# Optimization experiments

Hardware: AMD Instinct MI355X
Metric: run time of the kernel (lower is better)

The kernel has to match this reference:

```python
import jax, jax.numpy as jnp
import numpy as np

D_MODEL, D_INNER, D_STATE, D_CONV, NHEADS, HEADDIM, CHUNK = 2048, 4096, 128, 4, 64, 64, 64
CONV_DIM = D_INNER + 2 * D_STATE  # 4352
D_IN_PROJ = 2 * D_INNER + 2 * D_STATE + NHEADS  # 8512
EPS = 1e-5

def setup_inputs() -> dict:
    key = jax.random.key(0)
    ks = jax.random.split(key, 8)
    B, L = 2, 4096
    return {
        'u': jax.random.normal(ks[0], (B, L, D_MODEL), jnp.float32),
        'W_in': jax.random.normal(ks[1], (D_IN_PROJ, D_MODEL), jnp.float32) * 0.02,
        'conv_w': jax.random.normal(ks[2], (CONV_DIM, D_CONV), jnp.float32) * 0.2,
        'conv_b': jax.random.normal(ks[3], (CONV_DIM,), jnp.float32) * 0.02,
        'dt_bias': jax.random.normal(ks[4], (NHEADS,), jnp.float32) * 0.5,
        'A_log': jax.random.normal(ks[5], (NHEADS,), jnp.float32) * 0.5,
        'D': jax.random.normal(ks[6], (NHEADS,), jnp.float32),
        'norm_w': jnp.ones((D_INNER,), jnp.float32),
        'W_out': jax.random.normal(ks[7], (D_MODEL, D_INNER), jnp.float32) * 0.02,
    }

def silu(x):
    return x * jax.nn.sigmoid(x)

def segsum(x):
    # x: (..., T) -> (..., T, T); out[..., i, j] = sum_{j < k <= i} x[..., k], -inf above diag
    T = x.shape[-1]
    xr = jnp.broadcast_to(x[..., None], x.shape + (T,))
    m1 = jnp.tril(jnp.ones((T, T), bool), -1)
    s = jnp.cumsum(jnp.where(m1, xr, 0.0), axis=-2)
    m0 = jnp.tril(jnp.ones((T, T), bool), 0)
    return jnp.where(m0, s, -jnp.inf)

def ssd(x, A, B, C, chunk):
    # x: (b,L,h,p)  A: (b,L,h)  B,C: (b,L,n) shared across heads
    b, L, h, p = x.shape
    c = L // chunk
    x = x.reshape(b, c, chunk, h, p)
    A = A.reshape(b, c, chunk, h).transpose(0, 3, 1, 2)  # b h c l
    B = B.reshape(b, c, chunk, -1)
    C = C.reshape(b, c, chunk, -1)
    A_cs = jnp.cumsum(A, axis=-1)
    Lmat = jnp.exp(segsum(A))  # (b,h,c,l,s)
    Y_diag = jnp.einsum('bcln,bcsn,bhcls,bcshp->bclhp', C, B, Lmat, x)
    decay_states = jnp.exp(A_cs[..., -1:] - A_cs)  # (b,h,c,l)
    states = jnp.einsum('bcln,bhcl,bclhp->bchpn', B, decay_states, x)
    states = jnp.concatenate([jnp.zeros_like(states[:, :1]), states], axis=1)
    A_last = jnp.pad(A_cs[..., -1], ((0, 0), (0, 0), (1, 0)))  # (b,h,c+1)
    decay_chunk = jnp.exp(segsum(A_last))  # (b,h,c+1,c+1)
    new_states = jnp.einsum('bhzc,bchpn->bzhpn', decay_chunk, states)
    states, final = new_states[:, :-1], new_states[:, -1]
    sdo = jnp.exp(A_cs)  # (b,h,c,l)
    Y_off = jnp.einsum('bcln,bchpn,bhcl->bclhp', C, states, sdo)
    return (Y_diag + Y_off).reshape(b, L, h, p), final

def reference(u, W_in, conv_w, conv_b, dt_bias, A_log, D, norm_w, W_out):
    b, L, _ = u.shape
    zxbcdt = jnp.einsum('bld,ed->ble', u, W_in)
    z = zxbcdt[..., :D_INNER]
    xBC = zxbcdt[..., D_INNER:D_INNER + CONV_DIM]
    dt = jax.nn.softplus(zxbcdt[..., -NHEADS:] + dt_bias)  # (b,L,h)
    A = -jnp.exp(A_log)
    da_log = dt * A  # (b,L,h)
    # causal depthwise conv1d (kernel D_CONV, left pad D_CONV-1)
    xp = jnp.pad(xBC, ((0, 0), (D_CONV - 1, 0), (0, 0)))
    xBC = sum(xp[:, k:k + L, :] * conv_w[:, k] for k in range(D_CONV)) + conv_b
    xBC = silu(xBC)
    x = xBC[..., :D_INNER].reshape(b, L, NHEADS, HEADDIM)
    Bm = xBC[..., D_INNER:D_INNER + D_STATE]
    Cm = xBC[..., D_INNER + D_STATE:]
    y, final_state = ssd(x * dt[..., None], da_log, Bm, Cm, CHUNK)
    y = y + x * D[None, None, :, None]
    y = y.reshape(b, L, D_INNER)
    y = y * silu(z)
    y = y * jax.lax.rsqrt(jnp.mean(y * y, axis=-1, keepdims=True) + EPS) * norm_w
    return jnp.einsum('bld,ed->ble', y, W_out)
```

## Files before the change

### kernel.cpp

```cpp
#include <hip/hip_runtime.h>
#include <stdint.h>
#include <stddef.h>

#define SEQ     4096
#define DMODEL  2048
#define DINNER  4096
#define DSTATE  128
#define NH      64
#define HD      64
#define NCHUNK  64
#define CONVDIM 4352
#define DPROJ   8512

typedef __bf16 bf16_t;
typedef __bf16 bf16x8 __attribute__((ext_vector_type(8)));
typedef float  f32x4  __attribute__((ext_vector_type(4)));

__device__ __forceinline__ void async_cp16(const bf16_t* g, bf16_t* l) {
    __builtin_amdgcn_global_load_lds(
        (const __attribute__((address_space(1))) void*)g,
        (__attribute__((address_space(3))) void*)l,
        16, 0, 0);
}

__global__ __launch_bounds__(256) void zero_out_kernel(float* out, int n) {
    int i = blockIdx.x*256 + threadIdx.x;
    if (i < n) out[i] = 0.f;
}

__global__ void detect_kernel(const unsigned short* norm_w_raw, int* flag) {
    if (threadIdx.x == 0 && blockIdx.x == 0)
        *flag = (norm_w_raw[0] == 0x3F80) ? 1 : 0;
}

__global__ __launch_bounds__(256) void cast_kernel(
    const void* __restrict__ src, size_t elem_off, bf16_t* __restrict__ dst,
    int n, const int* __restrict__ flag)
{
    int i = blockIdx.x*256 + threadIdx.x;
    if (i >= n) return;
    if (*flag) dst[i] = ((const bf16_t*)src)[elem_off + i];
    else       dst[i] = (bf16_t)(((const float*)src)[elem_off + i]);
}

__device__ __forceinline__ void stage_half(
    const bf16_t* __restrict__ G, int grow0, int gmaxrow, int gld,
    int kt, bf16_t* lplane, int half, int tid)
{
    #pragma unroll
    for (int q = 0; q < 2; q++) {
        int rloc = half*128 + q*64 + (tid >> 3);
        int grow = grow0 + rloc; if (grow > gmaxrow) grow = gmaxrow;
        int gcol = kt + ((((tid & 7) ^ (rloc & 7))) << 3);
        async_cp16(G + (size_t)grow*gld + gcol, lplane + rloc*64 + ((tid & 7) << 3));
    }
}

#define GMM_READ_A(PLANE, KS)                                                  \
    _Pragma("unroll")                                                          \
    for (int m_ = 0; m_ < 8; m_++) {                                           \
        const int rl_ = wmBase + m_*16 + lrow;                                 \
        afr[m_] = *(const bf16x8*)((PLANE) + rl_*64 + ((((KS)*4+quad) ^ (rl_&7))<<3)); \
    }

#define GMM_READ_B(PLANE, KS, DST)                                             \
    _Pragma("unroll")                                                          \
    for (int n_ = 0; n_ < 4; n_++) {                                           \
        const int rl_ = wnBase + n_*16 + lrow;                                 \
        DST[n_] = *(const bf16x8*)((PLANE) + rl_*64 + ((((KS)*4+quad) ^ (rl_&7))<<3)); \
    }

#define GMM_TAIL(BKARR, NA, NB)                                                \
    __builtin_amdgcn_s_barrier();                                              \
    asm volatile("s_waitcnt lgkmcnt(0)" ::: "memory");                         \
    __builtin_amdgcn_sched_barrier(0);                                         \
    __builtin_amdgcn_s_setprio(1);                                             \
    _Pragma("unroll")                                                          \
    for (int m_ = 0; m_ < 8; m_++) {                                           \
        acc[m_][NA] = __builtin_amdgcn_mfma_f32_16x16x32_bf16(afr[m_], BKARR[NA], acc[m_][NA], 0,0,0); \
        acc[m_][NB] = __builtin_amdgcn_mfma_f32_16x16x32_bf16(afr[m_], BKARR[NB], acc[m_][NB], 0,0,0); \
    }                                                                          \
    __builtin_amdgcn_s_setprio(0);

template <typename OT>
__global__ __launch_bounds__(512, 2) void gemm256_kernel(
    const bf16_t* __restrict__ A, const bf16_t* __restrict__ W,
    OT* __restrict__ C, int M, int N, int K, int lda)
{
    extern __shared__ __align__(16) bf16_t lds[];
    bf16_t* lAa = lds;
    bf16_t* lAb = lds + 16384;
    bf16_t* lBa = lds + 32768;
    bf16_t* lBb = lds + 49152;

    const int tid  = threadIdx.x;
    const int lane = tid & 63;
    const int wid  = tid >> 6;
    const int lrow = lane & 15;
    const int quad = lane >> 4;
    const int wmBase = (wid >> 2) * 128;
    const int wnBase = (wid & 3) * 64;

    int wg = blockIdx.x;
    const int nwg = gridDim.x;
    if ((nwg & 7) == 0) { int cpx = nwg >> 3; wg = (wg & 7)*cpx + (wg >> 3); }
    const int ntx = (N + 255) >> 8;
    const int n0 = (wg % ntx) * 256;
    const int m0 = (wg / ntx) * 256;

    const int NT   = K >> 6;
    const int NTm1 = NT - 1;
    const int NT2  = NT >> 1;

    f32x4 acc[8][4] = {};
    bf16x8 afr[8], bk0[4], bk1[4];

    stage_half(A, m0, M-1, lda, 0,  lAa, 0, tid);
    stage_half(A, m0, M-1, lda, 0,  lAa, 1, tid);
    stage_half(W, n0, N-1, K,   0,  lBa, 0, tid);
    stage_half(W, n0, N-1, K,   0,  lBa, 1, tid);
    stage_half(A, m0, M-1, lda, 64, lAb, 0, tid);
    asm volatile("s_waitcnt vmcnt(2)" ::: "memory");
    __builtin_amdgcn_s_barrier();

    for (int i = 0; i < NT2; i++) {
        const int ktb = (2*i + 1) * 64;
        const int ktc = ((2*i + 2) & NTm1) * 64;
        const int ktd = ((2*i + 3) & NTm1) * 64;

        GMM_READ_A(lAa, 0)
        GMM_READ_B(lBa, 0, bk0)
        stage_half(A, m0, M-1, lda, ktb, lAb, 1, tid);
        GMM_TAIL(bk0, 0, 1)
        __builtin_amdgcn_s_barrier();
        GMM_READ_B(lBa, 1, bk1)
        stage_half(W, n0, N-1, K, ktb, lBb, 0, tid);
        GMM_TAIL(bk0, 2, 3)
        __builtin_amdgcn_s_barrier();
        GMM_READ_A(lAa, 1)
        stage_half(W, n0, N-1, K, ktb, lBb, 1, tid);
        GMM_TAIL(bk1, 0, 1)
        __builtin_amdgcn_s_barrier();
        stage_half(A, m0, M-1, lda, ktc, lAa, 0, tid);
        GMM_TAIL(bk1, 2, 3)
        asm volatile("s_waitcnt vmcnt(2)" ::: "memory");
        __builtin_amdgcn_s_barrier();

        GMM_READ_A(lAb, 0)
        GMM_READ_B(lBb, 0, bk0)
        stage_half(A, m0, M-1, lda, ktc, lAa, 1, tid);
        GMM_TAIL(bk0, 0, 1)
        __builtin_amdgcn_s_barrier();
        GMM_READ_B(lBb, 1, bk1)
        stage_half(W, n0, N-1, K, ktc, lBa, 0, tid);
        GMM_TAIL(bk0, 2, 3)
        __builtin_amdgcn_s_barrier();
        GMM_READ_A(lAb, 1)
        stage_half(W, n0, N-1, K, ktc, lBa, 1, tid);
        GMM_TAIL(bk1, 0, 1)
        __builtin_amdgcn_s_barrier();
        stage_half(A, m0, M-1, lda, ktd, lAb, 0, tid);
        GMM_TAIL(bk1, 2, 3)
        asm volatile("s_waitcnt vmcnt(2)" ::: "memory");
        __builtin_amdgcn_s_barrier();
    }

    asm volatile("s_waitcnt vmcnt(0)" ::: "memory");

    #pragma unroll
    for (int m = 0; m < 8; m++) {
        const int row = m0 + wmBase + m*16 + quad*4;
        #pragma unroll
        for (int n = 0; n < 4; n++) {
            const int col = n0 + wnBase + n*16 + lrow;
            if (col < N) {
                #pragma unroll
                for (int rr = 0; rr < 4; rr++)
                    C[(size_t)(row + rr)*N + col] = (OT)acc[m][n][rr];
            }
        }
    }
}

__global__ __launch_bounds__(256) void dt_kernel(
    const bf16_t* __restrict__ zx, const bf16_t* __restrict__ dt_bias,
    float* __restrict__ dtb)
{
    int i = blockIdx.x*256 + threadIdx.x;
    int h = i & 63, row = i >> 6;
    float raw = (float)zx[(size_t)row*DPROJ + (DINNER + CONVDIM) + h] + (float)dt_bias[h];
    dtb[i] = (raw > 20.f) ? raw : log1pf(expf(raw));
}

__global__ void cumsum_kernel(
    const float* __restrict__ dtb, const bf16_t* __restrict__ A_log,
    float* __restrict__ Acs)
{
    int blk = blockIdx.x;
    int h = blk & 63, c = blk >> 6;
    int lane = threadIdx.x;
    float Ah = -expf((float)A_log[h]);
    size_t row = (size_t)c*64 + lane;
    float v = dtb[row*64 + h] * Ah;
    #pragma unroll
    for (int off = 1; off < 64; off <<= 1) {
        float t = __shfl_up(v, off, 64);
        if (lane >= off) v += t;
    }
    Acs[(size_t)blk*64 + lane] = v;
}

__global__ __launch_bounds__(256) void conv_kernel(
    const bf16_t* __restrict__ zx, const bf16_t* __restrict__ conv_w,
    const bf16_t* __restrict__ conv_b, bf16_t* __restrict__ xbc)
{
    int i = blockIdx.x*256 + threadIdx.x;
    int cb = i % (CONVDIM/8);
    int l  = i / (CONVDIM/8);
    int ch0 = cb*8;
    const bf16_t* src = zx + (size_t)l*DPROJ + DINNER + ch0;
    float acc[8];
    {
        bf16x8 bv = *(const bf16x8*)(conv_b + ch0);
        #pragma unroll
        for (int j = 0; j < 8; j++) acc[j] = (float)bv[j];
    }
    bf16x8 w4[4];
    #pragma unroll
    for (int t = 0; t < 4; t++) w4[t] = *(const bf16x8*)(conv_w + ch0*4 + t*8);
    #pragma unroll
    for (int k = 0; k < 4; k++) {
        int ll = l - 3 + k;
        if (ll >= 0) {
            bf16x8 v = *(const bf16x8*)(src + (ptrdiff_t)(k-3)*DPROJ);
            #pragma unroll
            for (int j = 0; j < 8; j++)
                acc[j] += (float)v[j] * (float)w4[(j*4+k)>>3][(j*4+k)&7];
        }
    }
    bf16x8 o;
    #pragma unroll
    for (int j = 0; j < 8; j++)
        o[j] = (bf16_t)(acc[j] / (1.f + expf(-acc[j])));
    *(bf16x8*)(xbc + (size_t)i*8) = o;
}

__global__ __launch_bounds__(256) void states_kernel(
    const bf16_t* __restrict__ xbc, const float* __restrict__ dtb,
    const float* __restrict__ Acs, bf16_t* __restrict__ states)
{
    __shared__ __align__(16) bf16_t XsT[64*64];
    __shared__ __align__(16) bf16_t BT[128*64];
    __shared__ float AcsS[64];
    __shared__ float scaleS[64];
    const int blk = blockIdx.x;
    const int h = blk & 63, c = blk >> 6;
    const int tid = threadIdx.x, lane = tid & 63, wid = tid >> 6;
    const size_t rowbase = (size_t)c*64;

    if (tid < 64) AcsS[tid] = Acs[(size_t)blk*64 + tid];
    __syncthreads();
    if (tid < 64) scaleS[tid] = dtb[(rowbase + tid)*64 + h] * expf(AcsS[63] - AcsS[tid]);
    __syncthreads();

    {
        bf16x8 xa[2], b0[2], b1[2];
        #pragma unroll
        for (int half = 0; half < 2; half++) {
            #pragma unroll
            for (int j = 0; j < 8; j++) {
                int l = wid*16 + half*8 + j;
                const bf16_t* rp = xbc + (rowbase + l)*CONVDIM;
                xa[half][j] = (bf16_t)((float)rp[h*64 + lane] * scaleS[l]);
                b0[half][j] = rp[DINNER + lane];
                b1[half][j] = rp[DINNER + 64 + lane];
            }
        }
        #pragma unroll
        for (int half = 0; half < 2; half++) {
            int cch = wid*2 + half;
            *(bf16x8*)(XsT + lane*64       + ((cch ^ (lane & 7))*8)) = xa[half];
            *(bf16x8*)(BT  + lane*64       + ((cch ^ (lane & 7))*8)) = b0[half];
            *(bf16x8*)(BT  + (lane+64)*64  + ((cch ^ (lane & 7))*8)) = b1[half];
        }
    }
    __syncthreads();

    const int lrow = lane & 15, quad = lane >> 4;
    const int waveM = (wid & 1) * 32;
    const int waveN = (wid >> 1) * 64;
    f32x4 acc[2][4] = {};
    #pragma unroll
    for (int ks = 0; ks < 2; ks++) {
        bf16x8 af[2], bfr[4];
        #pragma unroll
        for (int i = 0; i < 2; i++) {
            int p = waveM + i*16 + lrow;
            af[i] = *(const bf16x8*)(XsT + p*64 + (((ks*4 + quad) ^ (p & 7))*8));
        }
        #pragma unroll
        for (int j = 0; j < 4; j++) {
            int n = waveN + j*16 + lrow;
            bfr[j] = *(const bf16x8*)(BT + n*64 + (((ks*4 + quad) ^ (n & 7))*8));
        }
        #pragma unroll
        for (int i = 0; i < 2; i++)
            #pragma unroll
            for (int j = 0; j < 4; j++)
                acc[i][j] = __builtin_amdgcn_mfma_f32_16x16x32_bf16(af[i], bfr[j], acc[i][j], 0, 0, 0);
    }

    const size_t sbase = (size_t)blk*8192;
    #pragma unroll
    for (int i = 0; i < 2; i++)
        #pragma unroll
        for (int j = 0; j < 4; j++) {
            int n = waveN + j*16 + lrow;
            #pragma unroll
            for (int r = 0; r < 4; r++) {
                int p = waveM + i*16 + quad*4 + r;
                states[sbase + (size_t)p*128 + n] = (bf16_t)acc[i][j][r];
            }
        }
}

__global__ __launch_bounds__(256) void gmat_kernel(
    const bf16_t* __restrict__ xbc, float* __restrict__ Gt)
{
    __shared__ __align__(16) float Ct[128*64];
    __shared__ __align__(16) float Bs2[64*128];
    int c = blockIdx.x;
    int tid = threadIdx.x;
    size_t rowbase = (size_t)c*64;
    for (int e = tid; e < 8192; e += 256) {
        int l = e >> 7, n = e & 127;
        const bf16_t* rp = xbc + (rowbase + l)*CONVDIM + DINNER;
        Bs2[e] = (float)rp[n];
        Ct[n*64 + (l ^ (n & 63))] = (float)rp[128 + n];
    }
    __syncthreads();
    int l = tid & 63, s0 = (tid >> 6) * 16;
    float acc[16] = {};
    for (int n4 = 0; n4 < 128; n4 += 4) {
        float c0 = Ct[(n4+0)*64 + (l ^ ((n4+0) & 63))];
        float c1 = Ct[(n4+1)*64 + (l ^ ((n4+1) & 63))];
        float c2 = Ct[(n4+2)*64 + (l ^ ((n4+2) & 63))];
        float c3 = Ct[(n4+3)*64 + (l ^ ((n4+3) & 63))];
        #pragma unroll
        for (int j = 0; j < 16; j++) {
            f32x4 bv = *(const f32x4*)&Bs2[(s0+j)*128 + n4];
            acc[j] += c0*bv[0] + c1*bv[1] + c2*bv[2] + c3*bv[3];
        }
    }
    float* gp = Gt + (size_t)c*4096;
    #pragma unroll
    for (int j = 0; j < 16; j++) gp[l*64 + (s0+j)] = acc[j];
}

__global__ __launch_bounds__(256) void scan_kernel(
    bf16_t* __restrict__ states, const float* __restrict__ Acs)
{
    int i = blockIdx.x*256 + threadIdx.x;
    int n = i & 127, p = (i >> 7) & 63, h = i >> 13;
    size_t off = (size_t)h*8192 + (size_t)p*128 + n;
    const float* ac = Acs + (size_t)h*64 + 63;
    float S = 0.f;
    for (int c = 0; c < 64; c++) {
        float tmp = (float)states[off];
        states[off] = (bf16_t)S;
        S = expf(ac[(size_t)c*4096]) * S + tmp;
        off += (size_t)64*8192;
    }
}

__global__ __launch_bounds__(256) void y_kernel(
    const bf16_t* __restrict__ xbc, const float* __restrict__ dtb,
    const float* __restrict__ Acs, const float* __restrict__ Gt,
    const bf16_t* __restrict__ states, const bf16_t* __restrict__ Dvec,
    bf16_t* __restrict__ y)
{
    __shared__ __align__(16) bf16_t Cs[64*128];
    __shared__ __align__(16) bf16_t Ss[64*128];
    __shared__ __align__(16) bf16_t Wm[64*64];
    __shared__ __align__(16) bf16_t XdT[64*64];
    __shared__ float acsS[64];
    __shared__ float dtS[64];
    const int blk = blockIdx.x;
    const int h = blk & 63, c = blk >> 6;
    const int tid = threadIdx.x, lane = tid & 63, wid = tid >> 6;
    const size_t rowbase = (size_t)c*64;
    const size_t sbase = (size_t)blk*8192;

    if (tid < 64) {
        acsS[tid] = Acs[(size_t)blk*64 + tid];
        dtS[tid]  = dtb[(rowbase + tid)*64 + h];
    }
    __syncthreads();

    #pragma unroll
    for (int it = 0; it < 4; it++) {
        int q = wid*256 + it*64 + lane;
        int l = q >> 4;
        int cl = (q & 15) ^ (l & 7);
        async_cp16(xbc + (rowbase + l)*CONVDIM + DINNER + 128 + cl*8,
                   Cs + (size_t)(wid*256 + it*64)*8);
        async_cp16(states + sbase + (size_t)l*128 + cl*8,
                   Ss + (size_t)(wid*256 + it*64)*8);
    }

    {
        const float* gp = Gt + (size_t)c*4096;
        #pragma unroll
        for (int k = 0; k < 16; k++) {
            int e = k*256 + tid;
            int l = e >> 6, s = e & 63;
            float w = 0.f;
            if (s <= l) w = gp[e] * expf(acsS[l] - acsS[s]);
            Wm[l*64 + (((s >> 3) ^ (l & 7))*8) + (s & 7)] = (bf16_t)w;
        }
    }

    {
        bf16x8 xd[2];
        #pragma unroll
        for (int half = 0; half < 2; half++)
            #pragma unroll
            for (int j = 0; j < 8; j++) {
                int s = wid*16 + half*8 + j;
                xd[half][j] = (bf16_t)((float)xbc[(rowbase + s)*CONVDIM + h*64 + lane] * dtS[s]);
            }
        #pragma unroll
        for (int half = 0; half < 2; half++) {
            int cch = wid*2 + half;
            *(bf16x8*)(XdT + lane*64 + ((cch ^ (lane & 7))*8)) = xd[half];
        }
    }
    __syncthreads();

    const int lrow = lane & 15, quad = lane >> 4;
    const int waveM = (wid & 1) * 32;
    const int waveN = (wid >> 1) * 32;
    f32x4 acc[2][2] = {};

    #pragma unroll
    for (int ks = 0; ks < 4; ks++) {
        bf16x8 af[2], bfr[2];
        #pragma unroll
        for (int i = 0; i < 2; i++) {
            int l = waveM + i*16 + lrow;
            af[i] = *(const bf16x8*)(Cs + l*128 + (((ks*4 + quad) ^ (l & 7))*8));
        }
        #pragma unroll
        for (int j = 0; j < 2; j++) {
            int p = waveN + j*16 + lrow;
            bfr[j] = *(const bf16x8*)(Ss + p*128 + (((ks*4 + quad) ^ (p & 7))*8));
        }
        #pragma unroll
        for (int i = 0; i < 2; i++)
            #pragma unroll
            for (int j = 0; j < 2; j++)
                acc[i][j] = __builtin_amdgcn_mfma_f32_16x16x32_bf16(af[i], bfr[j], acc[i][j], 0, 0, 0);
    }

    #pragma unroll
    for (int i = 0; i < 2; i++)
        #pragma unroll
        for (int r = 0; r < 4; r++) {
            int l = waveM + i*16 + quad*4 + r;
            float el = expf(acsS[l]);
            #pragma unroll
            for (int j = 0; j < 2; j++)
                acc[i][j][r] *= el;
        }

    #pragma unroll
    for (int ks = 0; ks < 2; ks++) {
        bf16x8 af[2], bfr[2];
        #pragma unroll
        for (int i = 0; i < 2; i++) {
            int l = waveM + i*16 + lrow;
            af[i] = *(const bf16x8*)(Wm + l*64 + (((ks*4 + quad) ^ (l & 7))*8));
        }
        #pragma unroll
        for (int j = 0; j < 2; j++) {
            int p = waveN + j*16 + lrow;
            bfr[j] = *(const bf16x8*)(XdT + p*64 + (((ks*4 + quad) ^ (p & 7))*8));
        }
        #pragma unroll
        for (int i = 0; i < 2; i++)
            #pragma unroll
            for (int j = 0; j < 2; j++)
                acc[i][j] = __builtin_amdgcn_mfma_f32_16x16x32_bf16(af[i], bfr[j], acc[i][j], 0, 0, 0);
    }

    const float Dh = (float)Dvec[h];
    #pragma unroll
    for (int i = 0; i < 2; i++)
        #pragma unroll
        for (int r = 0; r < 4; r++) {
            int l = waveM + i*16 + quad*4 + r;
            const bf16_t* xr = xbc + (rowbase + l)*CONVDIM + h*64;
            bf16_t* yr = y + (rowbase + l)*DPROJ + h*64;
            #pragma unroll
            for (int j = 0; j < 2; j++) {
                int p = waveN + j*16 + lrow;
                yr[p] = (bf16_t)(acc[i][j][r] + Dh * (float)xr[p]);
            }
        }
}

__global__ __launch_bounds__(256) void gatenorm_kernel(
    bf16_t* __restrict__ zx, const bf16_t* __restrict__ norm_w)
{
    __shared__ float red[4];
    int row = blockIdx.x;
    int tid = threadIdx.x;
    const bf16_t* zr = zx + (size_t)row*DPROJ;
    bf16_t* yr = zx + (size_t)row*DPROJ + DINNER;
    float vals[16]; float ss = 0.f;
    #pragma unroll
    for (int i = 0; i < 16; i++) {
        int e = i*256 + tid;
        float zv = (float)zr[e];
        float g = (float)yr[e] * (zv / (1.f + expf(-zv)));
        vals[i] = g; ss += g*g;
    }
    #pragma unroll
    for (int off = 32; off >= 1; off >>= 1) ss += __shfl_down(ss, off, 64);
    if ((tid & 63) == 0) red[tid >> 6] = ss;
    __syncthreads();
    float tot = red[0] + red[1] + red[2] + red[3];
    float scale = rsqrtf(tot * (1.f/4096.f) + 1e-5f);
    #pragma unroll
    for (int i = 0; i < 16; i++) {
        int e = i*256 + tid;
        yr[e] = (bf16_t)(vals[i] * scale * (float)norm_w[e]);
    }
}

extern "C" void kernel_launch(void* const* d_in, const int* in_sizes, int n_in,
                              void* d_out, int out_size, void* d_ws, size_t ws_size,
                              hipStream_t stream)
{
    const void* u_raw      = d_in[0];
    const void* W_in_raw   = d_in[1];
    const void* conv_w_raw = d_in[2];
    const void* conv_b_raw = d_in[3];
    const void* dt_b_raw   = d_in[4];
    const void* A_log_raw  = d_in[5];
    const void* D_raw      = d_in[6];
    const void* norm_w_raw = d_in[7];
    const void* W_out_raw  = d_in[8];
    float* out = (float*)d_out;

    const size_t SZ_HDR = 256 + 65536;
    const size_t SZ_ZX  = (size_t)SEQ*DPROJ*2;
    const size_t SZ_XBC = (size_t)SEQ*CONVDIM*2;
    const size_t SZ_ST  = (size_t)4096*8192*2;
    const size_t SZ_DTB = (size_t)SEQ*64*4;
    const size_t SZ_ACS = (size_t)4096*64*4;
    const size_t SZ_GT  = (size_t)64*4096*4;
    const size_t REQ = SZ_HDR + SZ_ZX + SZ_XBC + SZ_ST + SZ_DTB + SZ_ACS + SZ_GT;

    if (ws_size < REQ) {
        zero_out_kernel<<<(out_size + 255)/256, 256, 0, stream>>>(out, out_size);
        return;
    }

    static int smem_set = 0;
    if (!smem_set) {
        hipFuncSetAttribute(reinterpret_cast<const void*>(gemm256_kernel<bf16_t>),
                            hipFuncAttributeMaxDynamicSharedMemorySize, 131072);
        hipFuncSetAttribute(reinterpret_cast<const void*>(gemm256_kernel<float>),
                            hipFuncAttributeMaxDynamicSharedMemorySize, 131072);
        smem_set = 1;
    }

    char* w = (char*)d_ws;
    int*    flag   = (int*)w;            w += 256;
    bf16_t* smallb = (bf16_t*)w;         w += 65536;
    bf16_t* zx     = (bf16_t*)w;         w += SZ_ZX;
    bf16_t* xbc    = (bf16_t*)w;         w += SZ_XBC;
    bf16_t* states = (bf16_t*)w;         w += SZ_ST;
    float*  dtb    = (float*)w;          w += SZ_DTB;
    float*  Acs    = (float*)w;          w += SZ_ACS;
    float*  Gt     = (float*)w;          w += SZ_GT;
    bf16_t* yb     = zx + DINNER;

    bf16_t* conv_w_b  = smallb;
    bf16_t* conv_b_b  = smallb + 17408;
    bf16_t* dt_bias_b = smallb + 21760;
    bf16_t* A_log_b   = smallb + 21824;
    bf16_t* D_b       = smallb + 21888;
    bf16_t* norm_w_b  = smallb + 21952;
    bf16_t* u_b    = states;
    bf16_t* W_in_b = states + (size_t)SEQ*DMODEL;
    bf16_t* W_out_b = states;

    dim3 blk(256);
    detect_kernel<<<1, 1, 0, stream>>>((const unsigned short*)norm_w_raw, flag);
    cast_kernel<<<(17408+255)/256, blk, 0, stream>>>(conv_w_raw, 0, conv_w_b, 17408, flag);
    cast_kernel<<<(4352+255)/256,  blk, 0, stream>>>(conv_b_raw, 0, conv_b_b, 4352, flag);
    cast_kernel<<<1,               blk, 0, stream>>>(dt_b_raw,   0, dt_bias_b, 64, flag);
    cast_kernel<<<1,               blk, 0, stream>>>(A_log_raw,  0, A_log_b, 64, flag);
    cast_kernel<<<1,               blk, 0, stream>>>(D_raw,      0, D_b, 64, flag);
    cast_kernel<<<16,              blk, 0, stream>>>(norm_w_raw, 0, norm_w_b, 4096, flag);

    for (int b = 0; b < 2; b++) {
        float* outb = out + (size_t)b*SEQ*DMODEL;
        cast_kernel<<<32768, blk, 0, stream>>>(u_raw, (size_t)b*SEQ*DMODEL, u_b, SEQ*DMODEL, flag);
        cast_kernel<<<68096, blk, 0, stream>>>(W_in_raw, 0, W_in_b, DPROJ*DMODEL, flag);
        gemm256_kernel<bf16_t><<<dim3(34*16), dim3(512), 131072, stream>>>(
            u_b, W_in_b, zx, SEQ, DPROJ, DMODEL, DMODEL);
        dt_kernel<<<1024, blk, 0, stream>>>(zx, dt_bias_b, dtb);
        cumsum_kernel<<<4096, 64, 0, stream>>>(dtb, A_log_b, Acs);
        conv_kernel<<<8704, blk, 0, stream>>>(zx, conv_w_b, conv_b_b, xbc);
        states_kernel<<<4096, blk, 0, stream>>>(xbc, dtb, Acs, states);
        gmat_kernel<<<64, blk, 0, stream>>>(xbc, Gt);
        scan_kernel<<<2048, blk, 0, stream>>>(states, Acs);
        y_kernel<<<4096, blk, 0, stream>>>(xbc, dtb, Acs, Gt, states, D_b, yb);
        cast_kernel<<<32768, blk, 0, stream>>>(W_out_raw, 0, W_out_b, DMODEL*DINNER, flag);
        gatenorm_kernel<<<4096, blk, 0, stream>>>(zx, norm_w_b);
        gemm256_kernel<float><<<dim3(8*16), dim3(512), 131072, stream>>>(
            yb, W_out_b, outb, SEQ, DMODEL, DINNER, DPROJ);
    }
}
```

Before: 1.151 ms.

## Vectorize casts, split-K the output GEMM, and add partial LDS wait

The scalar cast kernels are replaced by a 4-wide vectorized cast, so each thread moves 16 bytes. The output projection GEMM, which had only 128 tiles, now splits K in two across 256 workgroups to fill more CUs. The second half goes to a float scratch buffer that reuses the xbc region, and a new add kernel sums it into the output. An early partial lgkmcnt wait is also inserted before the first MFMA tail, which may overlap LDS reads with compute; the split-K path costs extra global traffic for the partial sums.

Result: faster. 1.053 ms (-8.5%).

```diff
diff --git a/kernel.cpp b/kernel.cpp
--- a/kernel.cpp
+++ b/kernel.cpp
@@ -15,6 +15,7 @@
 typedef __bf16 bf16_t;
 typedef __bf16 bf16x8 __attribute__((ext_vector_type(8)));
 typedef float  f32x4  __attribute__((ext_vector_type(4)));
+typedef unsigned short u16x4 __attribute__((ext_vector_type(4)));
 
 __device__ __forceinline__ void async_cp16(const bf16_t* g, bf16_t* l) {
     __builtin_amdgcn_global_load_lds(
@@ -41,6 +42,35 @@
     if (i >= n) return;
     if (*flag) dst[i] = ((const bf16_t*)src)[elem_off + i];
     else       dst[i] = (bf16_t)(((const float*)src)[elem_off + i]);
+}
+
+__global__ __launch_bounds__(256) void cast4_kernel(
+    const void* __restrict__ src, size_t elem_off, bf16_t* __restrict__ dst,
+    int n4, const int* __restrict__ flag)
+{
+    int i = blockIdx.x*256 + threadIdx.x;
+    if (i >= n4) return;
+    if (*flag) {
+        u16x4 v = *(const u16x4*)((const unsigned short*)src + elem_off + (size_t)i*4);
+        *(u16x4*)(dst + (size_t)i*4) = v;
+    } else {
+        f32x4 v = *(const f32x4*)((const float*)src + elem_off + (size_t)i*4);
+        bf16_t o[4];
+        #pragma unroll
+        for (int j = 0; j < 4; j++) o[j] = (bf16_t)v[j];
+        *(u16x4*)(dst + (size_t)i*4) = *(const u16x4*)o;
+    }
+}
+
+__global__ __launch_bounds__(256) void addp_kernel(
+    float* __restrict__ out, const float* __restrict__ part, int n4)
+{
+    int i = blockIdx.x*256 + threadIdx.x;
+    if (i >= n4) return;
+    f32x4 a = *(const f32x4*)(out + (size_t)i*4);
+    f32x4 b = *(const f32x4*)(part + (size_t)i*4);
+    a[0]+=b[0]; a[1]+=b[1]; a[2]+=b[2]; a[3]+=b[3];
+    *(f32x4*)(out + (size_t)i*4) = a;
 }
 
 __device__ __forceinline__ void stage_half(
@@ -85,7 +115,7 @@
 template <typename OT>
 __global__ __launch_bounds__(512, 2) void gemm256_kernel(
     const bf16_t* __restrict__ A, const bf16_t* __restrict__ W,
-    OT* __restrict__ C, int M, int N, int K, int lda)
+    OT* C, OT* C2, int M, int N, int K, int lda, int khalf2)
 {
     extern __shared__ __align__(16) bf16_t lds[];
     bf16_t* lAa = lds;
@@ -104,11 +134,21 @@
     int wg = blockIdx.x;
     const int nwg = gridDim.x;
     if ((nwg & 7) == 0) { int cpx = nwg >> 3; wg = (wg & 7)*cpx + (wg >> 3); }
+
+    const int wld = K;
+    int kloc = K;
+    OT* Cw = C;
+    if (khalf2) {
+        const int htiles = nwg >> 1;
+        kloc = K >> 1;
+        if (wg >= htiles) { Cw = C2; wg -= htiles; A += kloc; W += kloc; }
+    }
+
     const int ntx = (N + 255) >> 8;
     const int n0 = (wg % ntx) * 256;
     const int m0 = (wg / ntx) * 256;
 
-    const int NT   = K >> 6;
+    const int NT   = kloc >> 6;
     const int NTm1 = NT - 1;
     const int NT2  = NT >> 1;
 
@@ -117,8 +157,8 @@
 
     stage_half(A, m0, M-1, lda, 0,  lAa, 0, tid);
     stage_half(A, m0, M-1, lda, 0,  lAa, 1, tid);
-    stage_half(W, n0, N-1, K,   0,  lBa, 0, tid);
-    stage_half(W, n0, N-1, K,   0,  lBa, 1, tid);
+    stage_half(W, n0, N-1, wld, 0,  lBa, 0, tid);
+    stage_half(W, n0, N-1, wld, 0,  lBa, 1, tid);
     stage_half(A, m0, M-1, lda, 64, lAb, 0, tid);
     asm volatile("s_waitcnt vmcnt(2)" ::: "memory");
     __builtin_amdgcn_s_barrier();
@@ -131,14 +171,15 @@
         GMM_READ_A(lAa, 0)
         GMM_READ_B(lBa, 0, bk0)
         stage_half(A, m0, M-1, lda, ktb, lAb, 1, tid);
+        asm volatile("s_waitcnt lgkmcnt(8)" ::: "memory");
         GMM_TAIL(bk0, 0, 1)
         __builtin_amdgcn_s_barrier();
         GMM_READ_B(lBa, 1, bk1)
-        stage_half(W, n0, N-1, K, ktb, lBb, 0, tid);
+        stage_half(W, n0, N-1, wld, ktb, lBb, 0, tid);
         GMM_TAIL(bk0, 2, 3)
         __builtin_amdgcn_s_barrier();
         GMM_READ_A(lAa, 1)
-        stage_half(W, n0, N-1, K, ktb, lBb, 1, tid);
+        stage_half(W, n0, N-1, wld, ktb, lBb, 1, tid);
         GMM_TAIL(bk1, 0, 1)
         __builtin_amdgcn_s_barrier();
         stage_half(A, m0, M-1, lda, ktc, lAa, 0, tid);
@@ -149,14 +190,15 @@
         GMM_READ_A(lAb, 0)
         GMM_READ_B(lBb, 0, bk0)
         stage_half(A, m0, M-1, lda, ktc, lAa, 1, tid);
+        asm volatile("s_waitcnt lgkmcnt(8)" ::: "memory");
         GMM_TAIL(bk0, 0, 1)
         __builtin_amdgcn_s_barrier();
         GMM_READ_B(lBb, 1, bk1)
-        stage_half(W, n0, N-1, K, ktc, lBa, 0, tid);
+        stage_half(W, n0, N-1, wld, ktc, lBa, 0, tid);
         GMM_TAIL(bk0, 2, 3)
         __builtin_amdgcn_s_barrier();
         GMM_READ_A(lAb, 1)
-        stage_half(W, n0, N-1, K, ktc, lBa, 1, tid);
+        stage_half(W, n0, N-1, wld, ktc, lBa, 1, tid);
         GMM_TAIL(bk1, 0, 1)
         __builtin_amdgcn_s_barrier();
         stage_half(A, m0, M-1, lda, ktd, lAb, 0, tid);
@@ -176,7 +218,7 @@
             if (col < N) {
                 #pragma unroll
                 for (int rr = 0; rr < 4; rr++)
-                    C[(size_t)(row + rr)*N + col] = (OT)acc[m][n][rr];
+                    Cw[(size_t)(row + rr)*N + col] = (OT)acc[m][n][rr];
             }
         }
     }
@@ -586,6 +628,7 @@
     float*  Acs    = (float*)w;          w += SZ_ACS;
     float*  Gt     = (float*)w;          w += SZ_GT;
     bf16_t* yb     = zx + DINNER;
+    float*  gpart  = (float*)xbc;
 
     bf16_t* conv_w_b  = smallb;
     bf16_t* conv_b_b  = smallb + 17408;
@@ -608,10 +651,10 @@
 
     for (int b = 0; b < 2; b++) {
         float* outb = out + (size_t)b*SEQ*DMODEL;
-        cast_kernel<<<32768, blk, 0, stream>>>(u_raw, (size_t)b*SEQ*DMODEL, u_b, SEQ*DMODEL, flag);
-        cast_kernel<<<68096, blk, 0, stream>>>(W_in_raw, 0, W_in_b, DPROJ*DMODEL, flag);
+        cast4_kernel<<<8192,  blk, 0, stream>>>(u_raw, (size_t)b*SEQ*DMODEL, u_b, SEQ*DMODEL/4, flag);
+        cast4_kernel<<<17024, blk, 0, stream>>>(W_in_raw, 0, W_in_b, DPROJ*DMODEL/4, flag);
         gemm256_kernel<bf16_t><<<dim3(34*16), dim3(512), 131072, stream>>>(
-            u_b, W_in_b, zx, SEQ, DPROJ, DMODEL, DMODEL);
+            u_b, W_in_b, zx, zx, SEQ, DPROJ, DMODEL, DMODEL, 0);
         dt_kernel<<<1024, blk, 0, stream>>>(zx, dt_bias_b, dtb);
         cumsum_kernel<<<4096, 64, 0, stream>>>(dtb, A_log_b, Acs);
         conv_kernel<<<8704, blk, 0, stream>>>(zx, conv_w_b, conv_b_b, xbc);
@@ -619,9 +662,10 @@
         gmat_kernel<<<64, blk, 0, stream>>>(xbc, Gt);
         scan_kernel<<<2048, blk, 0, stream>>>(states, Acs);
         y_kernel<<<4096, blk, 0, stream>>>(xbc, dtb, Acs, Gt, states, D_b, yb);
-        cast_kernel<<<32768, blk, 0, stream>>>(W_out_raw, 0, W_out_b, DMODEL*DINNER, flag);
+        cast4_kernel<<<8192, blk, 0, stream>>>(W_out_raw, 0, W_out_b, DMODEL*DINNER/4, flag);
         gatenorm_kernel<<<4096, blk, 0, stream>>>(zx, norm_w_b);
-        gemm256_kernel<float><<<dim3(8*16), dim3(512), 131072, stream>>>(
-            yb, W_out_b, outb, SEQ, DMODEL, DINNER, DPROJ);
-    }
-}
+        gemm256_kernel<float><<<dim3(2*8*16), dim3(512), 131072, stream>>>(
+            yb, W_out_b, outb, gpart, SEQ, DMODEL, DINNER, DPROJ, 1);
+        addp_kernel<<<8192, blk, 0, stream>>>(outb, gpart, SEQ*DMODEL/4);
+    }
+}
```
